# Optimization experiments

Hardware: AMD Instinct MI355X
Metric: run time of the kernel (lower is better)

## Reference

```python
import jax, jax.numpy as jnp
import numpy as np


def setup_inputs() -> dict:
    key = jax.random.key(0)
    ks = jax.random.split(key, 7)
    E = 768; CH = 3; PS = 16; B = 128; P = 196
    return {
        "x": jax.random.normal(ks[0], (B, P, E), dtype=jnp.float32),
        "We": jax.random.normal(ks[1], (CH * PS * PS, E), dtype=jnp.float32) * (1.0 / np.sqrt(E)),
        "be": jax.random.normal(ks[2], (CH * PS * PS,), dtype=jnp.float32) * 0.01,
        "filter_re": jax.random.normal(ks[3], (1, 1, 1, PS, PS), dtype=jnp.float32),
        "filter_im": jax.random.normal(ks[4], (1, 1, 1, PS, PS), dtype=jnp.float32),
        "Wd": jax.random.normal(ks[5], (E, CH * PS * PS), dtype=jnp.float32) * (1.0 / np.sqrt(CH * PS * PS)),
        "bd": jax.random.normal(ks[6], (E,), dtype=jnp.float32) * 0.01,
        "ch": 3,
        "patch_size": 16,
    }


def reference(x, We, be, filter_re, filter_im, Wd, bd, ch, patch_size):
    # encode: [b,p,E] -> [b,p,ch*ps*ps]
    h = jnp.einsum('bpe,ce->bpc', x, We) + be
    b, p, _ = h.shape
    h = h.reshape(b, p, ch, patch_size, patch_size)
    # batched 2D FFT over the two trailing patch dims
    hf = jnp.fft.fft2(h, axes=(-2, -1))
    filt = (filter_re + 1j * filter_im).astype(hf.dtype)  # [1,1,1,ps,ps]
    r = jnp.fft.ifft2(hf * filt, axes=(-2, -1))
    a = jnp.abs(r).reshape(b, p, ch * patch_size * patch_size)
    # decode: [b,p,ch*ps*ps] -> [b,p,E]
    return jnp.einsum('bpc,ec->bpe', a, Wd) + bd
```

## Files before the change

kernel.cpp:

```cpp
#include <hip/hip_runtime.h>

typedef short short8 __attribute__((ext_vector_type(8)));
typedef unsigned short ushort8 __attribute__((ext_vector_type(8)));
typedef float f32x4 __attribute__((ext_vector_type(4)));

__device__ __forceinline__ unsigned short f32_to_bf16(float f) {
  unsigned u = __float_as_uint(f);
  unsigned r = 0x7fffu + ((u >> 16) & 1u);
  return (unsigned short)((u + r) >> 16);
}
__device__ __forceinline__ float bf16_to_f32(unsigned short h) {
  return __uint_as_float(((unsigned)h) << 16);
}

__global__ void cvt_f32_bf16(const float* __restrict__ s,
                             unsigned short* __restrict__ d, int n8) {
  int i = blockIdx.x * blockDim.x + threadIdx.x;
  if (i >= n8) return;
  const float4* sp = (const float4*)s;
  float4 a = sp[2 * i], b = sp[2 * i + 1];
  ushort8 o;
  o[0] = f32_to_bf16(a.x); o[1] = f32_to_bf16(a.y);
  o[2] = f32_to_bf16(a.z); o[3] = f32_to_bf16(a.w);
  o[4] = f32_to_bf16(b.x); o[5] = f32_to_bf16(b.y);
  o[6] = f32_to_bf16(b.z); o[7] = f32_to_bf16(b.w);
  ((ushort8*)d)[i] = o;
}

__device__ __forceinline__ void gload_lds16(const void* g, void* l) {
  auto* gp = (const __attribute__((address_space(1))) uint32_t*)((uintptr_t)g);
  auto* lp = (__attribute__((address_space(3))) uint32_t*)(uint32_t)(uintptr_t)l;
  __builtin_amdgcn_global_load_lds(gp, lp, 16, 0, 0);
}

constexpr float C16T[16] = {
    1.f,  0.9238795325112867f,  0.7071067811865476f,  0.3826834323650898f,
    0.f, -0.3826834323650898f, -0.7071067811865476f, -0.9238795325112867f,
   -1.f, -0.9238795325112867f, -0.7071067811865476f, -0.3826834323650898f,
    0.f,  0.3826834323650898f,  0.7071067811865476f,  0.9238795325112867f};
constexpr float S16T[16] = {
    0.f,  0.3826834323650898f,  0.7071067811865476f,  0.9238795325112867f,
    1.f,  0.9238795325112867f,  0.7071067811865476f,  0.3826834323650898f,
    0.f, -0.3826834323650898f, -0.7071067811865476f, -0.9238795325112867f,
   -1.f, -0.9238795325112867f, -0.7071067811865476f, -0.3826834323650898f};

__device__ __forceinline__ void dft16(const float* xr, const float* xi,
                                      float* Xr, float* Xi, const float sgn) {
  float Tr[4][4], Ti[4][4];
#pragma unroll
  for (int c0 = 0; c0 < 4; ++c0) {
    float ar = xr[c0],      ai = xi[c0];
    float br = xr[c0 + 4],  bi = xi[c0 + 4];
    float cr = xr[c0 + 8],  ci = xi[c0 + 8];
    float dr = xr[c0 + 12], di = xi[c0 + 12];
    float Er = ar + cr, Ei = ai + ci, Fr = ar - cr, Fi = ai - ci;
    float Gr = br + dr, Gi = bi + di, Hr = br - dr, Hi = bi - di;
    Tr[c0][0] = Er + Gr; Ti[c0][0] = Ei + Gi;
    Tr[c0][2] = Er - Gr; Ti[c0][2] = Ei - Gi;
    float wHr = -sgn * Hi, wHi = sgn * Hr;
    Tr[c0][1] = Fr + wHr; Ti[c0][1] = Fi + wHi;
    Tr[c0][3] = Fr - wHr; Ti[c0][3] = Fi - wHi;
  }
#pragma unroll
  for (int u = 0; u < 16; ++u) {
    const int m = u & 3;
    float sr = Tr[0][m], si = Ti[0][m];
#pragma unroll
    for (int c0 = 1; c0 < 4; ++c0) {
      const int k = (u * c0) & 15;
      const float wr = C16T[k];
      const float wi = sgn * S16T[k];
      sr += wr * Tr[c0][m] - wi * Ti[c0][m];
      si += wr * Ti[c0][m] + wi * Tr[c0][m];
    }
    Xr[u] = sr; Xi[u] = si;
  }
}

__global__ __launch_bounds__(256) void fold_filter(
    const float* __restrict__ We, const float* __restrict__ be,
    const float* __restrict__ fre, const float* __restrict__ fim,
    unsigned short* __restrict__ Wre, unsigned short* __restrict__ Wim,
    float* __restrict__ be_re, float* __restrict__ be_im) {
  __shared__ float2 S[16 * 276];
  const int tid = threadIdx.x;
  const int p = tid >> 4;
  const int q = tid & 15;
  const int item = blockIdx.x * 16 + p;
  const bool isW = item < 2304;
  const bool isB = (item >= 2304) && (item < 2307);
  const int e = isW ? (item / 3) : 0;
  const int ch = isW ? (item % 3) : (isB ? (item - 2304) : 0);
  const int sb = p * 276;

  {
    float xr[16], xi[16], Xr[16], Xi[16];
#pragma unroll
    for (int c = 0; c < 16; ++c) {
      const int crow = ch * 256 + q * 16 + c;
      xr[c] = isW ? We[(size_t)crow * 768 + e] : be[crow];
      xi[c] = 0.f;
    }
    dft16(xr, xi, Xr, Xi, -1.f);
#pragma unroll
    for (int u = 0; u < 16; ++u) S[sb + q * 17 + u] = make_float2(Xr[u], Xi[u]);
  }
  __syncthreads();

  {
    float xr[16], xi[16], Xr[16], Xi[16];
#pragma unroll
    for (int k = 0; k < 16; ++k) {
      float2 t = S[sb + k * 17 + q];
      xr[k] = t.x; xi[k] = t.y;
    }
    dft16(xr, xi, Xr, Xi, -1.f);
#pragma unroll
    for (int v = 0; v < 16; ++v) {
      float fr = fre[v * 16 + q], fi = fim[v * 16 + q];
      float tr = Xr[v] * fr - Xi[v] * fi;
      float ti = Xr[v] * fi + Xi[v] * fr;
      xr[v] = tr; xi[v] = ti;
    }
    dft16(xr, xi, Xr, Xi, 1.f);
#pragma unroll
    for (int r = 0; r < 16; ++r) S[sb + r * 17 + q] = make_float2(Xr[r], Xi[r]);
  }
  __syncthreads();

  {
    float xr[16], xi[16], Xr[16], Xi[16];
#pragma unroll
    for (int u = 0; u < 16; ++u) {
      float2 t = S[sb + q * 17 + u];
      xr[u] = t.x; xi[u] = t.y;
    }
    dft16(xr, xi, Xr, Xi, 1.f);
#pragma unroll
    for (int c = 0; c < 16; ++c) {
      const int crow = ch * 256 + q * 16 + c;
      const float rr = Xr[c] * (1.f / 256.f);
      const float ri = Xi[c] * (1.f / 256.f);
      if (isW) {
        Wre[(size_t)crow * 768 + e] = f32_to_bf16(rr);
        Wim[(size_t)crow * 768 + e] = f32_to_bf16(ri);
      } else if (isB) {
        be_re[crow] = rr;
        be_im[crow] = ri;
      }
    }
  }
}

__global__ __launch_bounds__(256) void gemm_enc_dual(
    const unsigned short* __restrict__ A, const unsigned short* __restrict__ Bre,
    const unsigned short* __restrict__ Bim, const float* __restrict__ be_re,
    const float* __restrict__ be_im, unsigned short* __restrict__ out,
    int M, int K, int nbx) {
  __shared__ __align__(16) unsigned short As[2][128 * 64];
  __shared__ __align__(16) unsigned short Rs[2][64 * 64];
  __shared__ __align__(16) unsigned short Is[2][64 * 64];

  const int tid = threadIdx.x;
  const int lane = tid & 63;
  const int wid = tid >> 6;
  const int wr = wid >> 1, wc = wid & 1;

  const int nwg = gridDim.x;
  const int cpx = nwg >> 3;
  const int bid = blockIdx.x;
  const int lid = (bid & 7) * cpx + (bid >> 3);
  const int m0 = (lid / nbx) * 128, n0 = (lid % nbx) * 64;

  const int lr8 = lane >> 3;
  const int swk = ((lane & 7) ^ lr8) * 8;

  f32x4 accr[4][2] = {};
  f32x4 acci[4][2] = {};

  auto STAGE = [&](int buf, int k0) {
#pragma unroll
    for (int c = 0; c < 4; ++c) {
      const int rowc = wid * 32 + c * 8;
      gload_lds16(A + (size_t)(m0 + rowc + lr8) * K + (k0 + swk),
                  &As[buf][rowc * 64]);
    }
#pragma unroll
    for (int c = 0; c < 2; ++c) {
      const int rowc = wid * 16 + c * 8;
      gload_lds16(Bre + (size_t)(n0 + rowc + lr8) * K + (k0 + swk),
                  &Rs[buf][rowc * 64]);
      gload_lds16(Bim + (size_t)(n0 + rowc + lr8) * K + (k0 + swk),
                  &Is[buf][rowc * 64]);
    }
  };

  const int rsel = lane & 15;
  auto COMPUTE = [&](int buf) {
#pragma unroll
    for (int ks = 0; ks < 2; ++ks) {
      const int kbyte = ks * 64 + (lane >> 4) * 16;
      short8 af[4], brf[2], bif[2];
#pragma unroll
      for (int m = 0; m < 4; ++m) {
        const int row = wr * 64 + m * 16 + rsel;
        af[m] = *(const short8*)((const char*)&As[buf][0] +
                                 row * 128 + (kbyte ^ ((row & 7) << 4)));
      }
#pragma unroll
      for (int n = 0; n < 2; ++n) {
        const int row = wc * 32 + n * 16 + rsel;
        brf[n] = *(const short8*)((const char*)&Rs[buf][0] +
                                  row * 128 + (kbyte ^ ((row & 7) << 4)));
        bif[n] = *(const short8*)((const char*)&Is[buf][0] +
                                  row * 128 + (kbyte ^ ((row & 7) << 4)));
      }
#pragma unroll
      for (int m = 0; m < 4; ++m)
#pragma unroll
        for (int n = 0; n < 2; ++n) {
          accr[m][n] = __builtin_amdgcn_mfma_f32_16x16x32_bf16(
              af[m], brf[n], accr[m][n], 0, 0, 0);
          acci[m][n] = __builtin_amdgcn_mfma_f32_16x16x32_bf16(
              af[m], bif[n], acci[m][n], 0, 0, 0);
        }
    }
  };

  const int nk = K >> 6;
  STAGE(0, 0);
  __syncthreads();
  int cur = 0;
  for (int t = 1; t < nk; ++t) {
    STAGE(cur ^ 1, t * 64);
    COMPUTE(cur);
    __syncthreads();
    cur ^= 1;
  }
  COMPUTE(cur);

  const int fr = lane & 15, fq = lane >> 4;
  const int N = 768;
#pragma unroll
  for (int n = 0; n < 2; ++n) {
    const int gcol = n0 + wc * 32 + n * 16 + fr;
    const float br = be_re[gcol], bi = be_im[gcol];
#pragma unroll
    for (int m = 0; m < 4; ++m) {
      const int grow = m0 + wr * 64 + m * 16 + fq * 4;
#pragma unroll
      for (int j = 0; j < 4; ++j) {
        const float re = accr[m][n][j] + br;
        const float im = acci[m][n][j] + bi;
        out[(size_t)(grow + j) * N + gcol] = f32_to_bf16(sqrtf(re * re + im * im));
      }
    }
  }
}

__global__ __launch_bounds__(256) void gemm_bt(
    const unsigned short* __restrict__ A, const unsigned short* __restrict__ B,
    const float* __restrict__ bias, float* __restrict__ out,
    int M, int N, int K, int nbx) {
  __shared__ __align__(16) unsigned short As[2][128 * 64];
  __shared__ __align__(16) unsigned short Bs[2][128 * 64];

  const int tid = threadIdx.x;
  const int lane = tid & 63;
  const int wid = tid >> 6;
  const int wr = wid >> 1, wc = wid & 1;

  const int nwg = gridDim.x;
  const int cpx = nwg >> 3;
  const int bid = blockIdx.x;
  const int lid = (bid & 7) * cpx + (bid >> 3);
  const int m0 = (lid / nbx) * 128, n0 = (lid % nbx) * 128;

  const int lr8 = lane >> 3;
  const int swk = ((lane & 7) ^ lr8) * 8;

  f32x4 acc[4][4] = {};

  auto STAGE = [&](int buf, int k0) {
#pragma unroll
    for (int c = 0; c < 4; ++c) {
      const int rowc = wid * 32 + c * 8;
      gload_lds16(A + (size_t)(m0 + rowc + lr8) * K + (k0 + swk),
                  &As[buf][rowc * 64]);
      gload_lds16(B + (size_t)(n0 + rowc + lr8) * K + (k0 + swk),
                  &Bs[buf][rowc * 64]);
    }
  };

  const int rsel = lane & 15;
  auto COMPUTE = [&](int buf) {
#pragma unroll
    for (int ks = 0; ks < 2; ++ks) {
      const int kbyte = ks * 64 + (lane >> 4) * 16;
      short8 af[4], bf[4];
#pragma unroll
      for (int m = 0; m < 4; ++m) {
        const int row = wr * 64 + m * 16 + rsel;
        af[m] = *(const short8*)((const char*)&As[buf][0] +
                                 row * 128 + (kbyte ^ ((row & 7) << 4)));
      }
#pragma unroll
      for (int n = 0; n < 4; ++n) {
        const int row = wc * 64 + n * 16 + rsel;
        bf[n] = *(const short8*)((const char*)&Bs[buf][0] +
                                 row * 128 + (kbyte ^ ((row & 7) << 4)));
      }
#pragma unroll
      for (int m = 0; m < 4; ++m)
#pragma unroll
        for (int n = 0; n < 4; ++n)
          acc[m][n] = __builtin_amdgcn_mfma_f32_16x16x32_bf16(
              af[m], bf[n], acc[m][n], 0, 0, 0);
    }
  };

  const int nk = K >> 6;
  STAGE(0, 0);
  __syncthreads();
  int cur = 0;
  for (int t = 1; t < nk; ++t) {
    STAGE(cur ^ 1, t * 64);
    COMPUTE(cur);
    __syncthreads();
    cur ^= 1;
  }
  COMPUTE(cur);

  const int fr = lane & 15, fq = lane >> 4;
#pragma unroll
  for (int n = 0; n < 4; ++n) {
    const int gcol = n0 + wc * 64 + n * 16 + fr;
    const float bv = bias[gcol];
#pragma unroll
    for (int m = 0; m < 4; ++m) {
      const int grow = m0 + wr * 64 + m * 16 + fq * 4;
#pragma unroll
      for (int j = 0; j < 4; ++j)
        out[(size_t)(grow + j) * N + gcol] = acc[m][n][j] + bv;
    }
  }
}

extern "C" void kernel_launch(void* const* d_in, const int* in_sizes, int n_in,
                              void* d_out, int out_size, void* d_ws,
                              size_t ws_size, hipStream_t stream) {
  const float* x   = (const float*)d_in[0];
  const float* We  = (const float*)d_in[1];
  const float* be  = (const float*)d_in[2];
  const float* fre = (const float*)d_in[3];
  const float* fim = (const float*)d_in[4];
  const float* Wd  = (const float*)d_in[5];
  const float* bd  = (const float*)d_in[6];

  const int E = 768, C = 768;
  const int nX = in_sizes[0];
  const int M  = nX / E;
  const int nW = E * C;

  char* w = (char*)d_ws;
  unsigned short* xb    = (unsigned short*)w;
  unsigned short* Wdb   = (unsigned short*)(w + (size_t)nX * 2);
  unsigned short* Wre   = Wdb + nW;
  unsigned short* Wim   = Wre + nW;
  float*          be_re = (float*)(Wim + nW);
  float*          be_im = be_re + C;
  unsigned short* hb    = (unsigned short*)(be_im + C);

  cvt_f32_bf16<<<(nX / 8 + 255) / 256, 256, 0, stream>>>(x, xb, nX / 8);
  cvt_f32_bf16<<<(nW / 8 + 255) / 256, 256, 0, stream>>>(Wd, Wdb, nW / 8);

  fold_filter<<<145, 256, 0, stream>>>(We, be, fre, fim, Wre, Wim, be_re, be_im);

  const int nbx1 = C / 64;
  gemm_enc_dual<<<nbx1 * (M / 128), 256, 0, stream>>>(xb, Wre, Wim, be_re,
                                                      be_im, hb, M, E, nbx1);

  const int nbx2 = E / 128;
  gemm_bt<<<nbx2 * (M / 128), 256, 0, stream>>>(hb, Wdb, bd, (float*)d_out, M,
                                                E, C, nbx2);
}
```

Before: 154.1 us.

## Interleave real/imag filtered weights into one matrix for single-B encoder GEMM

The filter-folding kernel now writes the real and imaginary folded weights into one packed B matrix, laid out as alternating 32-row blocks of real and imaginary rows. The encoder GEMM becomes a standard 128x128 tile GEMM over this 2C-wide matrix. Each warp's accumulator tile holds matching real and imaginary columns, so the magnitude can still be computed in the epilogue. This unifies the B staging and LDS layout and keeps the MFMA work per tile the same, in exchange for a more intricate index mapping between the packed rows and the output columns.

```diff
diff --git a/kernel.cpp b/kernel.cpp
--- a/kernel.cpp
+++ b/kernel.cpp
@@ -80,8 +80,8 @@
 __global__ __launch_bounds__(256) void fold_filter(
     const float* __restrict__ We, const float* __restrict__ be,
     const float* __restrict__ fre, const float* __restrict__ fim,
-    unsigned short* __restrict__ Wre, unsigned short* __restrict__ Wim,
-    float* __restrict__ be_re, float* __restrict__ be_im) {
+    unsigned short* __restrict__ Bpp, float* __restrict__ be_re,
+    float* __restrict__ be_im) {
   __shared__ float2 S[16 * 276];
   const int tid = threadIdx.x;
   const int p = tid >> 4;
@@ -142,8 +142,9 @@
       const float rr = Xr[c] * (1.f / 256.f);
       const float ri = Xi[c] * (1.f / 256.f);
       if (isW) {
-        Wre[(size_t)crow * 768 + e] = f32_to_bf16(rr);
-        Wim[(size_t)crow * 768 + e] = f32_to_bf16(ri);
+        const size_t rre = (size_t)(crow >> 5) * 64 + (crow & 31);
+        Bpp[(rre)*768 + e]      = f32_to_bf16(rr);
+        Bpp[(rre + 32)*768 + e] = f32_to_bf16(ri);
       } else if (isB) {
         be_re[crow] = rr;
         be_im[crow] = ri;
@@ -152,14 +153,12 @@
   }
 }
 
-__global__ __launch_bounds__(256) void gemm_enc_dual(
-    const unsigned short* __restrict__ A, const unsigned short* __restrict__ Bre,
-    const unsigned short* __restrict__ Bim, const float* __restrict__ be_re,
-    const float* __restrict__ be_im, unsigned short* __restrict__ out,
-    int M, int K, int nbx) {
+__global__ __launch_bounds__(256) void gemm_enc(
+    const unsigned short* __restrict__ A, const unsigned short* __restrict__ B,
+    const float* __restrict__ be_re, const float* __restrict__ be_im,
+    unsigned short* __restrict__ out, int M, int K, int nbx) {
   __shared__ __align__(16) unsigned short As[2][128 * 64];
-  __shared__ __align__(16) unsigned short Rs[2][64 * 64];
-  __shared__ __align__(16) unsigned short Is[2][64 * 64];
+  __shared__ __align__(16) unsigned short Bs[2][128 * 64];
 
   const int tid = threadIdx.x;
   const int lane = tid & 63;
@@ -170,13 +169,12 @@
   const int cpx = nwg >> 3;
   const int bid = blockIdx.x;
   const int lid = (bid & 7) * cpx + (bid >> 3);
-  const int m0 = (lid / nbx) * 128, n0 = (lid % nbx) * 64;
+  const int m0 = (lid / nbx) * 128, n0 = (lid % nbx) * 128;
 
   const int lr8 = lane >> 3;
   const int swk = ((lane & 7) ^ lr8) * 8;
 
-  f32x4 accr[4][2] = {};
-  f32x4 acci[4][2] = {};
+  f32x4 acc[4][4] = {};
 
   auto STAGE = [&](int buf, int k0) {
 #pragma unroll
@@ -184,14 +182,8 @@
       const int rowc = wid * 32 + c * 8;
       gload_lds16(A + (size_t)(m0 + rowc + lr8) * K + (k0 + swk),
                   &As[buf][rowc * 64]);
-    }
-#pragma unroll
-    for (int c = 0; c < 2; ++c) {
-      const int rowc = wid * 16 + c * 8;
-      gload_lds16(Bre + (size_t)(n0 + rowc + lr8) * K + (k0 + swk),
-                  &Rs[buf][rowc * 64]);
-      gload_lds16(Bim + (size_t)(n0 + rowc + lr8) * K + (k0 + swk),
-                  &Is[buf][rowc * 64]);
+      gload_lds16(B + (size_t)(n0 + rowc + lr8) * K + (k0 + swk),
+                  &Bs[buf][rowc * 64]);
     }
   };
 
@@ -200,7 +192,7 @@
 #pragma unroll
     for (int ks = 0; ks < 2; ++ks) {
       const int kbyte = ks * 64 + (lane >> 4) * 16;
-      short8 af[4], brf[2], bif[2];
+      short8 af[4], bf[4];
 #pragma unroll
       for (int m = 0; m < 4; ++m) {
         const int row = wr * 64 + m * 16 + rsel;
@@ -208,22 +200,17 @@
                                  row * 128 + (kbyte ^ ((row & 7) << 4)));
       }
 #pragma unroll
-      for (int n = 0; n < 2; ++n) {
-        const int row = wc * 32 + n * 16 + rsel;
-        brf[n] = *(const short8*)((const char*)&Rs[buf][0] +
-                                  row * 128 + (kbyte ^ ((row & 7) << 4)));
-        bif[n] = *(const short8*)((const char*)&Is[buf][0] +
-                                  row * 128 + (kbyte ^ ((row & 7) << 4)));
+      for (int n = 0; n < 4; ++n) {
+        const int row = wc * 64 + n * 16 + rsel;
+        bf[n] = *(const short8*)((const char*)&Bs[buf][0] +
+                                 row * 128 + (kbyte ^ ((row & 7) << 4)));
       }
 #pragma unroll
       for (int m = 0; m < 4; ++m)
 #pragma unroll
-        for (int n = 0; n < 2; ++n) {
-          accr[m][n] = __builtin_amdgcn_mfma_f32_16x16x32_bf16(
-              af[m], brf[n], accr[m][n], 0, 0, 0);
-          acci[m][n] = __builtin_amdgcn_mfma_f32_16x16x32_bf16(
-              af[m], bif[n], acci[m][n], 0, 0, 0);
-        }
+        for (int n = 0; n < 4; ++n)
+          acc[m][n] = __builtin_amdgcn_mfma_f32_16x16x32_bf16(
+              af[m], bf[n], acc[m][n], 0, 0, 0);
     }
   };
 
@@ -240,19 +227,20 @@
   COMPUTE(cur);
 
   const int fr = lane & 15, fq = lane >> 4;
-  const int N = 768;
+  const int cbase = (n0 + wc * 64) >> 1;
 #pragma unroll
   for (int n = 0; n < 2; ++n) {
-    const int gcol = n0 + wc * 32 + n * 16 + fr;
+    const int gcol = cbase + n * 16 + fr;
     const float br = be_re[gcol], bi = be_im[gcol];
 #pragma unroll
     for (int m = 0; m < 4; ++m) {
       const int grow = m0 + wr * 64 + m * 16 + fq * 4;
 #pragma unroll
       for (int j = 0; j < 4; ++j) {
-        const float re = accr[m][n][j] + br;
-        const float im = acci[m][n][j] + bi;
-        out[(size_t)(grow + j) * N + gcol] = f32_to_bf16(sqrtf(re * re + im * im));
+        const float re = acc[m][n][j] + br;
+        const float im = acc[m][n + 2][j] + bi;
+        out[(size_t)(grow + j) * 768 + gcol] =
+            f32_to_bf16(sqrtf(re * re + im * im));
       }
     }
   }
@@ -365,20 +353,19 @@
   char* w = (char*)d_ws;
   unsigned short* xb    = (unsigned short*)w;
   unsigned short* Wdb   = (unsigned short*)(w + (size_t)nX * 2);
-  unsigned short* Wre   = Wdb + nW;
-  unsigned short* Wim   = Wre + nW;
-  float*          be_re = (float*)(Wim + nW);
+  unsigned short* Bpp   = Wdb + nW;
+  float*          be_re = (float*)(Bpp + 2 * (size_t)nW);
   float*          be_im = be_re + C;
   unsigned short* hb    = (unsigned short*)(be_im + C);
 
   cvt_f32_bf16<<<(nX / 8 + 255) / 256, 256, 0, stream>>>(x, xb, nX / 8);
   cvt_f32_bf16<<<(nW / 8 + 255) / 256, 256, 0, stream>>>(Wd, Wdb, nW / 8);
 
-  fold_filter<<<145, 256, 0, stream>>>(We, be, fre, fim, Wre, Wim, be_re, be_im);
-
-  const int nbx1 = C / 64;
-  gemm_enc_dual<<<nbx1 * (M / 128), 256, 0, stream>>>(xb, Wre, Wim, be_re,
-                                                      be_im, hb, M, E, nbx1);
+  fold_filter<<<145, 256, 0, stream>>>(We, be, fre, fim, Bpp, be_re, be_im);
+
+  const int nbx1 = (2 * C) / 128;
+  gemm_enc<<<nbx1 * (M / 128), 256, 0, stream>>>(xb, Bpp, be_re, be_im, hb, M,
+                                                 E, nbx1);
 
   const int nbx2 = E / 128;
   gemm_bt<<<nbx2 * (M / 128), 256, 0, stream>>>(hb, Wdb, bd, (float*)d_out, M,
```

Measured after the change: 152.3 us. No clear change (-1.1%).
